# Optimization experiments

Measured on AMD Instinct MI355X. Metric: run time of the kernel, lower is better.

## Reference

```python
import jax, jax.numpy as jnp
import numpy as np

NHEAD = 8; DM = 512; DFF = 2048; L = 4; S = 1024; NTOK = 51; MLP = 256; CLASSES = 7
GH = 3; GHID = 64; GCLS = 5; ALPHA = 0.2
HD = DM // NHEAD

_ADJ = np.array([[0,1,0,0,0],[1,1,1,1,0],[1,0,1,0,1],[1,0,0,1,1],[0,0,1,1,1]], dtype=np.int32)


def setup_inputs():
    key = jax.random.key(0)
    ks = jax.random.split(key, 24)
    r = lambda k, s, sc=0.05: jax.random.normal(k, s, jnp.float32) * sc
    return {
        'x': jax.random.normal(ks[0], (5, S, NTOK), jnp.float32),
        'adj': jnp.asarray(_ADJ),
        'W_enc': r(ks[1], (NTOK, DM)), 'b_enc': jnp.zeros((DM,), jnp.float32),
        'cls_tok': r(ks[2], (1, 1, DM)),
        'pos_emb': r(ks[3], (S + 1, DM)),
        'Wq': r(ks[4], (L, DM, DM)), 'bq': jnp.zeros((L, DM), jnp.float32),
        'Wk': r(ks[5], (L, DM, DM)), 'bk': jnp.zeros((L, DM), jnp.float32),
        'Wv': r(ks[6], (L, DM, DM)), 'bv': jnp.zeros((L, DM), jnp.float32),
        'Wo': r(ks[7], (L, DM, DM)), 'bo': jnp.zeros((L, DM), jnp.float32),
        'W1': r(ks[8], (L, DM, DFF)), 'b1': jnp.zeros((L, DFF), jnp.float32),
        'W2': r(ks[9], (L, DFF, DM)), 'b2': jnp.zeros((L, DM), jnp.float32),
        'g1': jnp.ones((L, DM), jnp.float32), 'be1': jnp.zeros((L, DM), jnp.float32),
        'g2': jnp.ones((L, DM), jnp.float32), 'be2': jnp.zeros((L, DM), jnp.float32),
        'Wd1': r(ks[10], (DM, MLP)), 'bd1': jnp.zeros((MLP,), jnp.float32),
        'Wd2': r(ks[11], (MLP, CLASSES)), 'bd2': jnp.zeros((CLASSES,), jnp.float32),
        'Wg': r(ks[12], (GH, 3, GHID), 0.3), 'ag': r(ks[13], (GH, 2 * GHID), 0.3),
        'Wgo': r(ks[14], (GH * GHID, GCLS), 0.3), 'ago': r(ks[15], (2 * GCLS,), 0.3),
    }


def _layernorm(x, g, b, eps=1e-5):
    m = x.mean(-1, keepdims=True)
    v = ((x - m) ** 2).mean(-1, keepdims=True)
    return (x - m) * jax.lax.rsqrt(v + eps) * g + b


def _gat_attn_layer(h_in, W, a, mask):
    # standard pyGAT GraphAttentionLayer: e_ij = LeakyReLU(a1.h_i + a2.h_j)
    F = W.shape[1]
    h = h_in @ W                                                    # [N, F]
    e = jax.nn.leaky_relu((h @ a[:F])[:, None] + (h @ a[F:])[None, :], ALPHA)
    att = jax.nn.softmax(jnp.where(mask, e, -9e15), axis=-1)        # adjacency-masked softmax
    return att @ h


def _gat(xg, mask, Wg, ag, Wgo, ago):
    # xg: [5 nodes, 3 feats]; GH attention heads concatenated, then output layer
    heads = jax.vmap(lambda W, a: jax.nn.elu(_gat_attn_layer(xg, W, a, mask)))(Wg, ag)  # [GH,5,GHID]
    hcat = jnp.transpose(heads, (1, 0, 2)).reshape(xg.shape[0], GH * GHID)
    out = jax.nn.elu(_gat_attn_layer(hcat, Wgo, ago, mask))         # [5, GCLS]
    return jax.nn.log_softmax(out, axis=1)


def _forward(x, adj, params):
    (W_enc, b_enc, cls_tok, pos_emb, Wq, bq, Wk, bk, Wv, bv, Wo, bo,
     W1, b1, W2, b2, g1, be1, g2, be2, Wd1, bd1, Wd2, bd2, Wg, ag, Wgo, ago) = params
    mask = adj > 0
    # --- batched GAT: the source loops over T timesteps x 5 feature groups; here fully vectorized ---
    # x[:, :, :15] : batch(=5 nodes) x T x 15 -> [T*5groups, 5 nodes, 3]
    xg = x[:, :, :15].reshape(5, S, 5, 3)
    xg = jnp.transpose(xg, (1, 2, 0, 3)).reshape(S * 5, 5, 3)
    gat_out = jax.vmap(lambda g: _gat(g, mask, Wg, ag, Wgo, ago))(xg)
    gat_out = gat_out.reshape(S, 5, 5, GCLS)                        # [T, group, node, class]
    # --- transformer branch (eval mode: dropout = identity) ---
    h = x @ W_enc + b_enc                                           # [5, S, DM]
    h = jnp.concatenate([jnp.broadcast_to(cls_tok, (5, 1, DM)), h], axis=1)
    h = h + pos_emb[None]
    for i in range(L):
        q = (h @ Wq[i] + bq[i]).reshape(5, S + 1, NHEAD, HD)
        k = (h @ Wk[i] + bk[i]).reshape(5, S + 1, NHEAD, HD)
        v = (h @ Wv[i] + bv[i]).reshape(5, S + 1, NHEAD, HD)
        sc = jnp.einsum('bthd,bshd->bhts', q, k) / jnp.sqrt(jnp.float32(HD))
        att = jax.nn.softmax(sc, axis=-1)
        o = jnp.einsum('bhts,bshd->bthd', att, v).reshape(5, S + 1, DM) @ Wo[i] + bo[i]
        h = _layernorm(h + o, g1[i], be1[i])
        f = jax.nn.relu(h @ W1[i] + b1[i]) @ W2[i] + b2[i]
        h = _layernorm(h + f, g2[i], be2[i])
    cls = h[:, 0, :]                                                # lambda: x[:, 0, :]
    out = (cls @ Wd1 + bd1) @ Wd2 + bd2                             # no activation between dense layers (as in source)
    return out, gat_out


def reference(x, adj, W_enc, b_enc, cls_tok, pos_emb, Wq, bq, Wk, bk, Wv, bv, Wo, bo, W1, b1, W2, b2, g1, be1, g2, be2, Wd1, bd1, Wd2, bd2, Wg, ag, Wgo, ago):
    params = (W_enc, b_enc, cls_tok, pos_emb, Wq, bq, Wk, bk, Wv, bv, Wo, bo,
              W1, b1, W2, b2, g1, be1, g2, be2, Wd1, bd1, Wd2, bd2, Wg, ag, Wgo, ago)
    return _forward(x, adj, params)
```

## Files before the change

### kernel.cpp

```cpp
#include <hip/hip_runtime.h>
#include <hip/hip_bf16.h>
#include <math.h>

#define NBATCH 5
#define SEQ    1024
#define T      1025
#define ROWS   (NBATCH * T)
#define MP     5248
#define DM     512
#define DFF    2048
#define NHEAD  8
#define HD     64
#define NTOK   51
#define MLPDIM 256
#define NCLS   7
#define GH     3
#define GHID   64
#define GCLS   5
#define NGRAPH (SEQ * 5)
#define QKVN   1536
#define TPAD   1088

typedef __attribute__((ext_vector_type(8))) short bf16x8;
typedef __attribute__((ext_vector_type(4))) float f32x4;

#define GM_AS(p)  ((const __attribute__((address_space(1))) void*)(p))
#define LDS_AS(p) ((__attribute__((address_space(3))) void*)(p))

__device__ __forceinline__ unsigned short f2bf(float f) {
    unsigned int u = __float_as_uint(f);
    unsigned int r = (u + 0x7FFFu + ((u >> 16) & 1u)) >> 16;
    return (unsigned short)r;
}

__global__ __launch_bounds__(256) void wconv_kernel(
    const float* __restrict__ W, unsigned short* __restrict__ Wt, int K, int N,
    long dstride)
{
    const float* Wm = W + (size_t)blockIdx.z * K * N;
    unsigned short* Wo = Wt + (size_t)blockIdx.z * dstride;
    __shared__ float tile[32][33];
    int bx = blockIdx.x * 32;
    int by = blockIdx.y * 32;
    int tx = threadIdx.x & 31, ty = threadIdx.x >> 5;
    #pragma unroll
    for (int i = 0; i < 32; i += 8)
        tile[ty + i][tx] = Wm[(size_t)(by + ty + i) * N + bx + tx];
    __syncthreads();
    #pragma unroll
    for (int i = 0; i < 32; i += 8)
        Wo[(size_t)(bx + ty + i) * K + by + tx] = f2bf(tile[tx][ty + i]);
}

__global__ __launch_bounds__(512) void bconcat_kernel(
    const float* __restrict__ bq, const float* __restrict__ bk,
    const float* __restrict__ bv, float* __restrict__ bqkv)
{
    int i = blockIdx.x, t = threadIdx.x;
    bqkv[i * QKVN + t]        = bq[i * DM + t];
    bqkv[i * QKVN + 512 + t]  = bk[i * DM + t];
    bqkv[i * QKVN + 1024 + t] = bv[i * DM + t];
}

__global__ __launch_bounds__(256) void gemm_mfma(
    const unsigned short* __restrict__ A, const unsigned short* __restrict__ Bt,
    const float* __restrict__ bias, float* __restrict__ Cf,
    unsigned short* __restrict__ Cb, int N, int K, int relu)
{
    __shared__ unsigned short As[128 * 64];
    __shared__ unsigned short Bs[128 * 64];
    int tid = threadIdx.x;
    int l = tid & 63, w = tid >> 6;
    int wr = w & 1, wc = w >> 1;
    int mlane = l & 15, quad = l >> 4;
    int m0 = blockIdx.y * 128, n0 = blockIdx.x * 128;

    f32x4 acc[4][4] = {};

    for (int k0 = 0; k0 < K; k0 += 64) {
        __syncthreads();
        #pragma unroll
        for (int it = 0; it < 4; ++it) {
            int c = tid + it * 256;
            int row = c >> 3, cc = c & 7;
            const unsigned short* ga = A  + (size_t)(m0 + row) * K + k0 + cc * 8;
            __builtin_amdgcn_global_load_lds(GM_AS(ga), LDS_AS(As + c * 8), 16, 0, 0);
            const unsigned short* gb = Bt + (size_t)(n0 + row) * K + k0 + cc * 8;
            __builtin_amdgcn_global_load_lds(GM_AS(gb), LDS_AS(Bs + c * 8), 16, 0, 0);
        }
        __syncthreads();
        #pragma unroll
        for (int half = 0; half < 2; ++half) {
            int ko = half * 32 + quad * 8;
            bf16x8 afrag[4], bfrag[4];
            #pragma unroll
            for (int mi = 0; mi < 4; ++mi)
                afrag[mi] = *(const bf16x8*)(As + (wr * 64 + mi * 16 + mlane) * 64 + ko);
            #pragma unroll
            for (int ni = 0; ni < 4; ++ni)
                bfrag[ni] = *(const bf16x8*)(Bs + (wc * 64 + ni * 16 + mlane) * 64 + ko);
            #pragma unroll
            for (int mi = 0; mi < 4; ++mi)
                #pragma unroll
                for (int ni = 0; ni < 4; ++ni)
                    acc[mi][ni] = __builtin_amdgcn_mfma_f32_16x16x32_bf16(
                        afrag[mi], bfrag[ni], acc[mi][ni], 0, 0, 0);
        }
    }

    #pragma unroll
    for (int mi = 0; mi < 4; ++mi) {
        #pragma unroll
        for (int r = 0; r < 4; ++r) {
            int gm = m0 + wr * 64 + mi * 16 + quad * 4 + r;
            size_t rowoff = (size_t)gm * N;
            #pragma unroll
            for (int ni = 0; ni < 4; ++ni) {
                int gn = n0 + wc * 64 + ni * 16 + mlane;
                float val = acc[mi][ni][r] + bias[gn];
                if (relu) val = fmaxf(val, 0.f);
                if (Cb) Cb[rowoff + gn] = f2bf(val);
                else    Cf[rowoff + gn] = val;
            }
        }
    }
}

__global__ __launch_bounds__(256) void vtrans_kernel(
    const unsigned short* __restrict__ vb, unsigned short* __restrict__ vt, int qs)
{
    __shared__ unsigned short tile[64][72];
    int bh = blockIdx.y;
    int b = bh >> 3, h = bh & 7;
    int t0 = blockIdx.x * 64;
    int tid = threadIdx.x;
    #pragma unroll
    for (int it = 0; it < 2; ++it) {
        int c = tid + it * 256;
        int key = c >> 3, cc = c & 7;
        int gk = t0 + key; if (gk >= T) gk = T - 1;
        *(bf16x8*)(&tile[key][cc * 8]) =
            *(const bf16x8*)(vb + ((size_t)b * T + gk) * qs + h * HD + cc * 8);
    }
    __syncthreads();
    #pragma unroll
    for (int it = 0; it < 2; ++it) {
        int c = tid + it * 256;
        int d = c >> 3, cc = c & 7;
        unsigned short tmp[8];
        #pragma unroll
        for (int j = 0; j < 8; ++j) tmp[j] = tile[cc * 8 + j][d];
        *(bf16x8*)(vt + ((size_t)bh * 64 + d) * TPAD + t0 + cc * 8) = *(bf16x8*)tmp;
    }
}

#define AQT 64
#define NCH 17
__global__ __launch_bounds__(256) void attn_mfma(
    const unsigned short* __restrict__ qb, const unsigned short* __restrict__ kb,
    const unsigned short* __restrict__ vt, unsigned short* __restrict__ ob,
    int qs)
{
    __shared__ unsigned short Ks[64 * 72];
    __shared__ unsigned short Vs[64 * 72];
    __shared__ unsigned short Ps[4][16 * 72];
    int bh = blockIdx.y;
    int b = bh >> 3, h = bh & 7;
    int t0 = blockIdx.x * AQT;
    int tid = threadIdx.x;
    int l = tid & 63, w = tid >> 6;
    int ml = l & 15, quad = l >> 4;
    size_t rowbase = (size_t)b * T;
    const unsigned short* vtb = vt + (size_t)bh * 64 * TPAD;

    int qrow = t0 + w * 16 + ml; if (qrow >= T) qrow = T - 1;
    const unsigned short* qp = qb + (rowbase + qrow) * qs + h * HD + quad * 8;
    bf16x8 qf0 = *(const bf16x8*)qp;
    bf16x8 qf1 = *(const bf16x8*)(qp + 32);

    int c_a = tid, c_b = tid + 256;
    int rowa = c_a >> 3, cca = c_a & 7;
    int rowb = c_b >> 3, ccb = c_b & 7;

    f32x4 oacc[4] = {};
    float mrow[4] = {-1e30f, -1e30f, -1e30f, -1e30f};
    float lrow[4] = {0.f, 0.f, 0.f, 0.f};

    bf16x8 kra, krb, vra, vrb;
    {
        int gka = rowa;  int gkb = rowb;
        kra = *(const bf16x8*)(kb + (rowbase + gka) * qs + h * HD + cca * 8);
        krb = *(const bf16x8*)(kb + (rowbase + gkb) * qs + h * HD + ccb * 8);
        vra = *(const bf16x8*)(vtb + (size_t)rowa * TPAD + 0 + cca * 8);
        vrb = *(const bf16x8*)(vtb + (size_t)rowb * TPAD + 0 + ccb * 8);
    }

    for (int ch = 0; ch < NCH; ++ch) {
        int c0 = ch * 64;
        __syncthreads();
        *(bf16x8*)(Ks + rowa * 72 + cca * 8) = kra;
        *(bf16x8*)(Ks + rowb * 72 + ccb * 8) = krb;
        *(bf16x8*)(Vs + rowa * 72 + cca * 8) = vra;
        *(bf16x8*)(Vs + rowb * 72 + ccb * 8) = vrb;
        __syncthreads();
        if (ch + 1 < NCH) {
            int n0k = c0 + 64;
            int gka = n0k + rowa; if (gka >= T) gka = T - 1;
            int gkb = n0k + rowb; if (gkb >= T) gkb = T - 1;
            kra = *(const bf16x8*)(kb + (rowbase + gka) * qs + h * HD + cca * 8);
            krb = *(const bf16x8*)(kb + (rowbase + gkb) * qs + h * HD + ccb * 8);
            vra = *(const bf16x8*)(vtb + (size_t)rowa * TPAD + n0k + cca * 8);
            vrb = *(const bf16x8*)(vtb + (size_t)rowb * TPAD + n0k + ccb * 8);
        }

        f32x4 s[4] = {};
        #pragma unroll
        for (int ni = 0; ni < 4; ++ni) {
            bf16x8 kf0 = *(const bf16x8*)(Ks + (ni * 16 + ml) * 72 + quad * 8);
            bf16x8 kf1 = *(const bf16x8*)(Ks + (ni * 16 + ml) * 72 + 32 + quad * 8);
            s[ni] = __builtin_amdgcn_mfma_f32_16x16x32_bf16(qf0, kf0, s[ni], 0, 0, 0);
            s[ni] = __builtin_amdgcn_mfma_f32_16x16x32_bf16(qf1, kf1, s[ni], 0, 0, 0);
        }
        #pragma unroll
        for (int ni = 0; ni < 4; ++ni) {
            bool valid = (c0 + ni * 16 + ml) < T;
            #pragma unroll
            for (int r = 0; r < 4; ++r)
                s[ni][r] = valid ? s[ni][r] * 0.125f : -1e30f;
        }
        #pragma unroll
        for (int r = 0; r < 4; ++r) {
            float mx = fmaxf(fmaxf(s[0][r], s[1][r]), fmaxf(s[2][r], s[3][r]));
            #pragma unroll
            for (int off = 1; off < 16; off <<= 1)
                mx = fmaxf(mx, __shfl_xor(mx, off));
            float mnew = fmaxf(mrow[r], mx);
            float alpha = __expf(mrow[r] - mnew);
            mrow[r] = mnew;
            float rs = 0.f;
            #pragma unroll
            for (int ni = 0; ni < 4; ++ni) {
                float p = __expf(s[ni][r] - mnew);
                s[ni][r] = p; rs += p;
            }
            #pragma unroll
            for (int off = 1; off < 16; off <<= 1)
                rs += __shfl_xor(rs, off);
            lrow[r] = lrow[r] * alpha + rs;
            #pragma unroll
            for (int ni = 0; ni < 4; ++ni) oacc[ni][r] *= alpha;
        }
        unsigned short* pw = Ps[w];
        #pragma unroll
        for (int r = 0; r < 4; ++r)
            #pragma unroll
            for (int ni = 0; ni < 4; ++ni)
                pw[(quad * 4 + r) * 72 + ((ni * 16 + ml) ^ (quad << 4))] = f2bf(s[ni][r]);
        int sw = ((ml >> 2) & 3) << 4;
        #pragma unroll
        for (int kc = 0; kc < 2; ++kc) {
            bf16x8 pf = *(const bf16x8*)(pw + ml * 72 + ((kc * 32 + quad * 8) ^ sw));
            #pragma unroll
            for (int ni = 0; ni < 4; ++ni) {
                bf16x8 vf = *(const bf16x8*)(Vs + (ni * 16 + ml) * 72 + kc * 32 + quad * 8);
                oacc[ni] = __builtin_amdgcn_mfma_f32_16x16x32_bf16(pf, vf, oacc[ni], 0, 0, 0);
            }
        }
    }

    #pragma unroll
    for (int r = 0; r < 4; ++r) {
        int grow = t0 + w * 16 + quad * 4 + r;
        if (grow >= T) continue;
        float inv = 1.f / lrow[r];
        unsigned short* op = ob + (rowbase + grow) * DM + h * HD;
        #pragma unroll
        for (int ni = 0; ni < 4; ++ni)
            op[ni * 16 + ml] = f2bf(oacc[ni][r] * inv);
    }
}

__global__ __launch_bounds__(256) void encoder_kernel(
    const float* __restrict__ x, const float* __restrict__ W_enc,
    const float* __restrict__ b_enc, const float* __restrict__ cls_tok,
    const float* __restrict__ pos_emb, float* __restrict__ h,
    unsigned short* __restrict__ hb)
{
    int row = blockIdx.x;
    int b = row / T, tt = row % T;
    int tid = threadIdx.x;
    float* hp = h + (size_t)row * DM;
    unsigned short* hbp = hb + (size_t)row * DM;
    if (tt == 0) {
        float a0 = cls_tok[tid]       + pos_emb[tid];
        float a1 = cls_tok[tid + 256] + pos_emb[tid + 256];
        hp[tid] = a0; hp[tid + 256] = a1;
        hbp[tid] = f2bf(a0); hbp[tid + 256] = f2bf(a1);
        return;
    }
    __shared__ float xs[NTOK];
    int s = tt - 1;
    if (tid < NTOK) xs[tid] = x[((size_t)b * SEQ + s) * NTOK + tid];
    __syncthreads();
    #pragma unroll
    for (int rep = 0; rep < 2; ++rep) {
        int d = tid + rep * 256;
        float acc = b_enc[d] + pos_emb[(size_t)tt * DM + d];
        for (int kx = 0; kx < NTOK; ++kx) acc += xs[kx] * W_enc[kx * DM + d];
        hp[d] = acc;
        hbp[d] = f2bf(acc);
    }
}

__global__ __launch_bounds__(256) void add_ln_kernel(
    float* __restrict__ h, const float* __restrict__ r,
    const float* __restrict__ g, const float* __restrict__ be,
    unsigned short* __restrict__ hb)
{
    int w = threadIdx.x >> 6, l = threadIdx.x & 63;
    int row = blockIdx.x * 4 + w;
    if (row >= ROWS) return;
    float* hp = h + (size_t)row * DM + l * 8;
    const float* rp = r + (size_t)row * DM + l * 8;
    unsigned short* hbp = hb + (size_t)row * DM + l * 8;
    float4 a0 = *(const float4*)(hp);
    float4 a1 = *(const float4*)(hp + 4);
    float4 b0 = *(const float4*)(rp);
    float4 b1 = *(const float4*)(rp + 4);
    float v[8] = {a0.x + b0.x, a0.y + b0.y, a0.z + b0.z, a0.w + b0.w,
                  a1.x + b1.x, a1.y + b1.y, a1.z + b1.z, a1.w + b1.w};
    float s = 0.f;
    #pragma unroll
    for (int i = 0; i < 8; ++i) s += v[i];
    #pragma unroll
    for (int off = 1; off < 64; off <<= 1) s += __shfl_xor(s, off);
    float mean = s * (1.f / DM);
    float sq = 0.f;
    #pragma unroll
    for (int i = 0; i < 8; ++i) { v[i] -= mean; sq += v[i] * v[i]; }
    #pragma unroll
    for (int off = 1; off < 64; off <<= 1) sq += __shfl_xor(sq, off);
    float inv = rsqrtf(sq * (1.f / DM) + 1e-5f);
    float4 g0 = *(const float4*)(g + l * 8);
    float4 g1 = *(const float4*)(g + l * 8 + 4);
    float4 e0 = *(const float4*)(be + l * 8);
    float4 e1 = *(const float4*)(be + l * 8 + 4);
    float o[8];
    o[0] = v[0]*inv*g0.x + e0.x; o[1] = v[1]*inv*g0.y + e0.y;
    o[2] = v[2]*inv*g0.z + e0.z; o[3] = v[3]*inv*g0.w + e0.w;
    o[4] = v[4]*inv*g1.x + e1.x; o[5] = v[5]*inv*g1.y + e1.y;
    o[6] = v[6]*inv*g1.z + e1.z; o[7] = v[7]*inv*g1.w + e1.w;
    *(float4*)(hp)     = make_float4(o[0], o[1], o[2], o[3]);
    *(float4*)(hp + 4) = make_float4(o[4], o[5], o[6], o[7]);
    ushort4 p0 = {f2bf(o[0]), f2bf(o[1]), f2bf(o[2]), f2bf(o[3])};
    ushort4 p1 = {f2bf(o[4]), f2bf(o[5]), f2bf(o[6]), f2bf(o[7])};
    *(ushort4*)(hbp)     = p0;
    *(ushort4*)(hbp + 4) = p1;
}

__global__ __launch_bounds__(256) void dec1_kernel(
    const float* __restrict__ h, const float* __restrict__ Wd1,
    float* __restrict__ part)
{
    int kc = blockIdx.x, b = blockIdx.y, tid = threadIdx.x;
    __shared__ float cs[64];
    const float* cls = h + (size_t)b * T * DM;
    if (tid < 64) cs[tid] = cls[kc * 64 + tid];
    __syncthreads();
    float acc = 0.f;
    #pragma unroll
    for (int kx = 0; kx < 64; ++kx)
        acc += cs[kx] * Wd1[(size_t)(kc * 64 + kx) * MLPDIM + tid];
    part[(size_t)(b * 8 + kc) * MLPDIM + tid] = acc;
}

__global__ __launch_bounds__(256) void dec2_kernel(
    const float* __restrict__ part, const float* __restrict__ bd1,
    const float* __restrict__ Wd2, const float* __restrict__ bd2,
    float* __restrict__ out)
{
    __shared__ float t1s[MLPDIM];
    int tid = threadIdx.x;
    for (int b = 0; b < NBATCH; ++b) {
        float acc = bd1[tid];
        #pragma unroll
        for (int kc = 0; kc < 8; ++kc)
            acc += part[(size_t)(b * 8 + kc) * MLPDIM + tid];
        t1s[tid] = acc;
        __syncthreads();
        if (tid < NCLS) {
            float a2 = bd2[tid];
            for (int kx = 0; kx < MLPDIM; ++kx) a2 += t1s[kx] * Wd2[kx * NCLS + tid];
            out[b * NCLS + tid] = a2;
        }
        __syncthreads();
    }
}

__global__ __launch_bounds__(64) void gat_kernel(
    const float* __restrict__ x, const int* __restrict__ adj,
    const float* __restrict__ Wg, const float* __restrict__ ag,
    const float* __restrict__ Wgo, const float* __restrict__ ago,
    float* __restrict__ out)
{
    int g = blockIdx.x;
    int s = g / 5, jj = g % 5;
    int tid = threadIdx.x;
    __shared__ float xs[5][3];
    __shared__ int adjs[25];
    __shared__ float hb[GH][5][GHID];
    __shared__ float o1[GH][5][GHID];
    __shared__ float srcb[GH][5], dstb[GH][5];
    __shared__ float attb[GH][5][5];
    __shared__ float h2[5][5], src2[5], dst2[5], att2[5][5], o2[5][5];

    if (tid < 15) { int n = tid / 3, c = tid % 3;
        xs[n][c] = x[(size_t)n * SEQ * NTOK + (size_t)s * NTOK + jj * 3 + c]; }
    if (tid < 25) adjs[tid] = adj[tid];
    __syncthreads();

    #pragma unroll
    for (int hh = 0; hh < GH; ++hh)
        #pragma unroll
        for (int n = 0; n < 5; ++n)
            hb[hh][n][tid] = xs[n][0] * Wg[hh * 192 + tid]
                           + xs[n][1] * Wg[hh * 192 + 64 + tid]
                           + xs[n][2] * Wg[hh * 192 + 128 + tid];
    __syncthreads();

    if (tid < 15) { int hh = tid / 5, n = tid % 5; float a = 0.f;
        for (int f = 0; f < GHID; ++f) a += hb[hh][n][f] * ag[hh * 128 + f];
        srcb[hh][n] = a;
    } else if (tid >= 32 && tid < 47) { int t2 = tid - 32; int hh = t2 / 5, n = t2 % 5; float a = 0.f;
        for (int f = 0; f < GHID; ++f) a += hb[hh][n][f] * ag[hh * 128 + 64 + f];
        dstb[hh][n] = a;
    }
    __syncthreads();

    if (tid < 15) { int hh = tid / 5, i = tid % 5;
        float e[5]; float mx = -1e30f;
        #pragma unroll
        for (int j2 = 0; j2 < 5; ++j2) {
            float ev = srcb[hh][i] + dstb[hh][j2];
            ev = ev > 0.f ? ev : 0.2f * ev;
            e[j2] = ev;
            if (adjs[i * 5 + j2] && ev > mx) mx = ev;
        }
        float sum = 0.f;
        #pragma unroll
        for (int j2 = 0; j2 < 5; ++j2) {
            float p = adjs[i * 5 + j2] ? expf(e[j2] - mx) : 0.f;
            e[j2] = p; sum += p;
        }
        float inv = 1.f / sum;
        #pragma unroll
        for (int j2 = 0; j2 < 5; ++j2) attb[hh][i][j2] = e[j2] * inv;
    }
    __syncthreads();

    #pragma unroll
    for (int hh = 0; hh < GH; ++hh)
        #pragma unroll
        for (int n = 0; n < 5; ++n) {
            float a = 0.f;
            #pragma unroll
            for (int j2 = 0; j2 < 5; ++j2) a += attb[hh][n][j2] * hb[hh][j2][tid];
            o1[hh][n][tid] = a > 0.f ? a : expm1f(a);
        }
    __syncthreads();

    if (tid < 25) { int n = tid / 5, m = tid % 5; float a = 0.f;
        for (int hh = 0; hh < GH; ++hh)
            for (int f = 0; f < GHID; ++f)
                a += o1[hh][n][f] * Wgo[(hh * GHID + f) * GCLS + m];
        h2[n][m] = a;
    }
    __syncthreads();

    if (tid < 5) { float a = 0.f;
        for (int m = 0; m < GCLS; ++m) a += h2[tid][m] * ago[m];
        src2[tid] = a;
    } else if (tid >= 8 && tid < 13) { int n = tid - 8; float a = 0.f;
        for (int m = 0; m < GCLS; ++m) a += h2[n][m] * ago[GCLS + m];
        dst2[n] = a;
    }
    __syncthreads();

    if (tid < 5) { int i = tid;
        float e[5]; float mx = -1e30f;
        #pragma unroll
        for (int j2 = 0; j2 < 5; ++j2) {
            float ev = src2[i] + dst2[j2];
            ev = ev > 0.f ? ev : 0.2f * ev;
            e[j2] = ev;
            if (adjs[i * 5 + j2] && ev > mx) mx = ev;
        }
        float sum = 0.f;
        #pragma unroll
        for (int j2 = 0; j2 < 5; ++j2) {
            float p = adjs[i * 5 + j2] ? expf(e[j2] - mx) : 0.f;
            e[j2] = p; sum += p;
        }
        float inv = 1.f / sum;
        #pragma unroll
        for (int j2 = 0; j2 < 5; ++j2) att2[i][j2] = e[j2] * inv;
    }
    __syncthreads();

    if (tid < 25) { int n = tid / 5, m = tid % 5; float a = 0.f;
        #pragma unroll
        for (int j2 = 0; j2 < 5; ++j2) a += att2[n][j2] * h2[j2][m];
        o2[n][m] = a > 0.f ? a : expm1f(a);
    }
    __syncthreads();

    if (tid < 5) { int n = tid;
        float mx = o2[n][0];
        #pragma unroll
        for (int m = 1; m < GCLS; ++m) mx = fmaxf(mx, o2[n][m]);
        float sum = 0.f;
        #pragma unroll
        for (int m = 0; m < GCLS; ++m) sum += expf(o2[n][m] - mx);
        float ls = logf(sum);
        #pragma unroll
        for (int m = 0; m < GCLS; ++m)
            out[(size_t)g * 25 + n * 5 + m] = o2[n][m] - mx - ls;
    }
}

extern "C" void kernel_launch(void* const* d_in, const int* in_sizes, int n_in,
                              void* d_out, int out_size, void* d_ws, size_t ws_size,
                              hipStream_t stream)
{
    const float* x       = (const float*)d_in[0];
    const int*   adj     = (const int*)  d_in[1];
    const float* W_enc   = (const float*)d_in[2];
    const float* b_enc   = (const float*)d_in[3];
    const float* cls_tok = (const float*)d_in[4];
    const float* pos_emb = (const float*)d_in[5];
    const float* Wq = (const float*)d_in[6];
    const float* bq = (const float*)d_in[7];
    const float* Wk = (const float*)d_in[8];
    const float* bk = (const float*)d_in[9];
    const float* Wv = (const float*)d_in[10];
    const float* bv = (const float*)d_in[11];
    const float* Wo = (const float*)d_in[12];
    const float* bo = (const float*)d_in[13];
    const float* W1 = (const float*)d_in[14];
    const float* b1 = (const float*)d_in[15];
    const float* W2 = (const float*)d_in[16];
    const float* b2 = (const float*)d_in[17];
    const float* g1 = (const float*)d_in[18];
    const float* be1= (const float*)d_in[19];
    const float* g2 = (const float*)d_in[20];
    const float* be2= (const float*)d_in[21];
    const float* Wd1= (const float*)d_in[22];
    const float* bd1= (const float*)d_in[23];
    const float* Wd2= (const float*)d_in[24];
    const float* bd2= (const float*)d_in[25];
    const float* Wg = (const float*)d_in[26];
    const float* ag = (const float*)d_in[27];
    const float* Wgo= (const float*)d_in[28];
    const float* ago= (const float*)d_in[29];
    float* out = (float*)d_out;

    float* ws = (float*)d_ws;
    float* h = ws;
    float* q = h + (size_t)MP * DM;
    unsigned short* hb   = (unsigned short*)(q + (size_t)MP * DM);
    unsigned short* qkvb = hb + (size_t)MP * DM;
    unsigned short* ob   = qkvb + (size_t)MP * QKVN;
    unsigned short* f1b  = qkvb;
    unsigned short* Wqkvt= ob + (size_t)MP * DM;
    unsigned short* Wot  = Wqkvt + (size_t)4 * QKVN * DM;
    unsigned short* W1t  = Wot + (size_t)4 * DM * DM;
    unsigned short* W2t  = W1t + (size_t)4 * DM * DFF;
    float* bqkv = (float*)(W2t + (size_t)4 * DFF * DM);
    float* dpart = bqkv + 4 * QKVN;
    unsigned short* vt = (unsigned short*)(dpart + NBATCH * 8 * MLPDIM);

    const long QS = (long)QKVN * DM;
    wconv_kernel<<<dim3(DM/32,  DM/32,  4), 256, 0, stream>>>(Wq, Wqkvt,            DM,  DM, QS);
    wconv_kernel<<<dim3(DM/32,  DM/32,  4), 256, 0, stream>>>(Wk, Wqkvt + 512*512,  DM,  DM, QS);
    wconv_kernel<<<dim3(DM/32,  DM/32,  4), 256, 0, stream>>>(Wv, Wqkvt + 1024*512, DM,  DM, QS);
    wconv_kernel<<<dim3(DM/32,  DM/32,  4), 256, 0, stream>>>(Wo, Wot, DM,  DM, (long)DM*DM);
    wconv_kernel<<<dim3(DFF/32, DM/32,  4), 256, 0, stream>>>(W1, W1t, DM,  DFF, (long)DM*DFF);
    wconv_kernel<<<dim3(DM/32,  DFF/32, 4), 256, 0, stream>>>(W2, W2t, DFF, DM, (long)DFF*DM);
    bconcat_kernel<<<4, 512, 0, stream>>>(bq, bk, bv, bqkv);

    gat_kernel<<<NGRAPH, 64, 0, stream>>>(x, adj, Wg, ag, Wgo, ago, out + NBATCH * NCLS);
    encoder_kernel<<<ROWS, 256, 0, stream>>>(x, W_enc, b_enc, cls_tok, pos_emb, h, hb);

    dim3 g512 (DM  / 128, MP / 128);
    dim3 gqkv (QKVN / 128, MP / 128);
    dim3 g2048(DFF / 128, MP / 128);
    dim3 gAttn(TPAD / AQT, NBATCH * NHEAD);
    dim3 gVt  (TPAD / 64, NBATCH * NHEAD);
    int gLN = (ROWS + 3) / 4;

    for (int i = 0; i < 4; ++i) {
        gemm_mfma<<<gqkv, 256, 0, stream>>>(hb, Wqkvt + (size_t)i*QKVN*DM, bqkv + i*QKVN, nullptr, qkvb, QKVN, DM, 0);
        vtrans_kernel<<<gVt, 256, 0, stream>>>(qkvb + 1024, vt, QKVN);
        attn_mfma<<<gAttn, 256, 0, stream>>>(qkvb, qkvb + 512, vt, ob, QKVN);
        gemm_mfma<<<g512, 256, 0, stream>>>(ob, Wot + (size_t)i*DM*DM, bo + i*DM, q, nullptr, DM, DM, 0);
        add_ln_kernel<<<gLN, 256, 0, stream>>>(h, q, g1 + i*DM, be1 + i*DM, hb);
        gemm_mfma<<<g2048, 256, 0, stream>>>(hb,  W1t + (size_t)i*DM*DFF, b1 + i*DFF, nullptr, f1b, DFF, DM, 1);
        gemm_mfma<<<g512, 256, 0, stream>>>(f1b, W2t + (size_t)i*DM*DFF, b2 + i*DM,  q, nullptr, DM, DFF, 0);
        add_ln_kernel<<<gLN, 256, 0, stream>>>(h, q, g2 + i*DM, be2 + i*DM, hb);
    }

    dec1_kernel<<<dim3(8, NBATCH), 256, 0, stream>>>(h, Wd1, dpart);
    dec2_kernel<<<1, 256, 0, stream>>>(dpart, bd1, Wd2, bd2, out);
}
```

Before: 957.7 us.

## Split attention over two key-range halves and merge partials in combine kernel

Attention blocks now split the key chunks into two halves along a new grid dimension. Each half writes unnormalized bf16 partial outputs plus per-row running max and sum, and a new combine kernel merges them with the log-sum-exp rescaling. The aim is to double the attention grid (17x40 blocks grows to 17x40x2) so more CUs are busy on the 256-CU part. The cost is an extra launch, extra global traffic for partials, and an extra bf16 rounding of the unnormalized partials.

```diff
diff --git a/kernel.cpp b/kernel.cpp
--- a/kernel.cpp
+++ b/kernel.cpp
@@ -32,6 +32,9 @@
     unsigned int r = (u + 0x7FFFu + ((u >> 16) & 1u)) >> 16;
     return (unsigned short)r;
 }
+__device__ __forceinline__ float bf2f(unsigned short u) {
+    return __uint_as_float((unsigned int)u << 16);
+}
 
 __global__ __launch_bounds__(256) void wconv_kernel(
     const float* __restrict__ W, unsigned short* __restrict__ Wt, int K, int N,
@@ -158,8 +161,8 @@
 #define NCH 17
 __global__ __launch_bounds__(256) void attn_mfma(
     const unsigned short* __restrict__ qb, const unsigned short* __restrict__ kb,
-    const unsigned short* __restrict__ vt, unsigned short* __restrict__ ob,
-    int qs)
+    const unsigned short* __restrict__ vt,
+    unsigned short* __restrict__ opart, float* __restrict__ mlpart, int qs)
 {
     __shared__ unsigned short Ks[64 * 72];
     __shared__ unsigned short Vs[64 * 72];
@@ -167,6 +170,9 @@
     int bh = blockIdx.y;
     int b = bh >> 3, h = bh & 7;
     int t0 = blockIdx.x * AQT;
+    int sp = blockIdx.z;
+    int chbeg = sp ? 9 : 0;
+    int chend = sp ? NCH : 9;
     int tid = threadIdx.x;
     int l = tid & 63, w = tid >> 6;
     int ml = l & 15, quad = l >> 4;
@@ -188,14 +194,16 @@
 
     bf16x8 kra, krb, vra, vrb;
     {
-        int gka = rowa;  int gkb = rowb;
+        int c0 = chbeg * 64;
+        int gka = c0 + rowa; if (gka >= T) gka = T - 1;
+        int gkb = c0 + rowb; if (gkb >= T) gkb = T - 1;
         kra = *(const bf16x8*)(kb + (rowbase + gka) * qs + h * HD + cca * 8);
         krb = *(const bf16x8*)(kb + (rowbase + gkb) * qs + h * HD + ccb * 8);
-        vra = *(const bf16x8*)(vtb + (size_t)rowa * TPAD + 0 + cca * 8);
-        vrb = *(const bf16x8*)(vtb + (size_t)rowb * TPAD + 0 + ccb * 8);
-    }
-
-    for (int ch = 0; ch < NCH; ++ch) {
+        vra = *(const bf16x8*)(vtb + (size_t)rowa * TPAD + c0 + cca * 8);
+        vrb = *(const bf16x8*)(vtb + (size_t)rowb * TPAD + c0 + ccb * 8);
+    }
+
+    for (int ch = chbeg; ch < chend; ++ch) {
         int c0 = ch * 64;
         __syncthreads();
         *(bf16x8*)(Ks + rowa * 72 + cca * 8) = kra;
@@ -203,7 +211,7 @@
         *(bf16x8*)(Vs + rowa * 72 + cca * 8) = vra;
         *(bf16x8*)(Vs + rowb * 72 + ccb * 8) = vrb;
         __syncthreads();
-        if (ch + 1 < NCH) {
+        if (ch + 1 < chend) {
             int n0k = c0 + 64;
             int gka = n0k + rowa; if (gka >= T) gka = T - 1;
             int gkb = n0k + rowb; if (gkb >= T) gkb = T - 1;
@@ -268,16 +276,48 @@
         }
     }
 
+    int pbase = (sp * 40 + bh) * TPAD;
     #pragma unroll
     for (int r = 0; r < 4; ++r) {
         int grow = t0 + w * 16 + quad * 4 + r;
         if (grow >= T) continue;
-        float inv = 1.f / lrow[r];
-        unsigned short* op = ob + (rowbase + grow) * DM + h * HD;
+        unsigned short* op = opart + (size_t)(pbase + grow) * 64;
         #pragma unroll
         for (int ni = 0; ni < 4; ++ni)
-            op[ni * 16 + ml] = f2bf(oacc[ni][r] * inv);
-    }
+            op[ni * 16 + ml] = f2bf(oacc[ni][r]);
+        if (ml == 0) {
+            mlpart[(size_t)(pbase + grow) * 2]     = mrow[r];
+            mlpart[(size_t)(pbase + grow) * 2 + 1] = lrow[r];
+        }
+    }
+}
+
+__global__ __launch_bounds__(256) void attn_combine(
+    const unsigned short* __restrict__ opart, const float* __restrict__ mlpart,
+    unsigned short* __restrict__ ob)
+{
+    int qt = blockIdx.x, bh = blockIdx.y;
+    int b = bh >> 3, h = bh & 7;
+    int tid = threadIdx.x;
+    int ql = tid >> 2, dg = tid & 3;
+    int q = qt * 64 + ql;
+    if (q >= T) return;
+    int base0 = bh * TPAD + q;
+    int base1 = (40 + bh) * TPAD + q;
+    float m0 = mlpart[(size_t)base0 * 2], l0 = mlpart[(size_t)base0 * 2 + 1];
+    float m1 = mlpart[(size_t)base1 * 2], l1 = mlpart[(size_t)base1 * 2 + 1];
+    float M = fmaxf(m0, m1);
+    float w0 = __expf(m0 - M), w1 = __expf(m1 - M);
+    float inv = 1.f / (l0 * w0 + l1 * w1);
+    const unsigned short* p0 = opart + (size_t)base0 * 64 + dg * 16;
+    const unsigned short* p1 = opart + (size_t)base1 * 64 + dg * 16;
+    unsigned short* op = ob + ((size_t)b * T + q) * DM + h * HD + dg * 16;
+    unsigned short res[16];
+    #pragma unroll
+    for (int i = 0; i < 16; ++i)
+        res[i] = f2bf((bf2f(p0[i]) * w0 + bf2f(p1[i]) * w1) * inv);
+    *(bf16x8*)(op)     = *(bf16x8*)(res);
+    *(bf16x8*)(op + 8) = *(bf16x8*)(res + 8);
 }
 
 __global__ __launch_bounds__(256) void encoder_kernel(
@@ -578,6 +618,8 @@
     float* bqkv = (float*)(W2t + (size_t)4 * DFF * DM);
     float* dpart = bqkv + 4 * QKVN;
     unsigned short* vt = (unsigned short*)(dpart + NBATCH * 8 * MLPDIM);
+    unsigned short* opart = vt + (size_t)40 * 64 * TPAD;
+    float* mlpart = (float*)(opart + (size_t)2 * 40 * TPAD * 64);
 
     const long QS = (long)QKVN * DM;
     wconv_kernel<<<dim3(DM/32,  DM/32,  4), 256, 0, stream>>>(Wq, Wqkvt,            DM,  DM, QS);
@@ -594,14 +636,16 @@
     dim3 g512 (DM  / 128, MP / 128);
     dim3 gqkv (QKVN / 128, MP / 128);
     dim3 g2048(DFF / 128, MP / 128);
-    dim3 gAttn(TPAD / AQT, NBATCH * NHEAD);
+    dim3 gAttn(TPAD / AQT, NBATCH * NHEAD, 2);
+    dim3 gComb(TPAD / 64, NBATCH * NHEAD);
     dim3 gVt  (TPAD / 64, NBATCH * NHEAD);
     int gLN = (ROWS + 3) / 4;
 
     for (int i = 0; i < 4; ++i) {
         gemm_mfma<<<gqkv, 256, 0, stream>>>(hb, Wqkvt + (size_t)i*QKVN*DM, bqkv + i*QKVN, nullptr, qkvb, QKVN, DM, 0);
         vtrans_kernel<<<gVt, 256, 0, stream>>>(qkvb + 1024, vt, QKVN);
-        attn_mfma<<<gAttn, 256, 0, stream>>>(qkvb, qkvb + 512, vt, ob, QKVN);
+        attn_mfma<<<gAttn, 256, 0, stream>>>(qkvb, qkvb + 512, vt, opart, mlpart, QKVN);
+        attn_combine<<<gComb, 256, 0, stream>>>(opart, mlpart, ob);
         gemm_mfma<<<g512, 256, 0, stream>>>(ob, Wot + (size_t)i*DM*DM, bo + i*DM, q, nullptr, DM, DM, 0);
         add_ln_kernel<<<gLN, 256, 0, stream>>>(h, q, g1 + i*DM, be1 + i*DM, hb);
         gemm_mfma<<<g2048, 256, 0, stream>>>(hb,  W1t + (size_t)i*DM*DFF, b1 + i*DFF, nullptr, f1b, DFF, DM, 1);
```

Result: slower. 984.0 us (+2.7%).

## Split-K the narrow GEMMs into bf16 partials reduced in LayerNorm; drop online softmax max

Applied to the files above, without the earlier changes.

The Wo and W2 projections (N=512, only 4x41 tiles) now run as split-K GEMMs (2 and 4 slices) that write bf16 partial sums. The add+LayerNorm kernel reduces those partials and adds the bias, which removes the fp32 intermediate buffer. Attention also drops the running-max rescaling and just sums exp(s) directly, with the row-sum reduction deferred to the end. This adds parallelism for the underfilled GEMMs and cuts softmax work, but rounds partials to bf16 and risks exp overflow on large scores.

```diff
diff --git a/kernel.cpp b/kernel.cpp
--- a/kernel.cpp
+++ b/kernel.cpp
@@ -32,6 +32,9 @@
     unsigned int r = (u + 0x7FFFu + ((u >> 16) & 1u)) >> 16;
     return (unsigned short)r;
 }
+__device__ __forceinline__ float bf2f(unsigned short u) {
+    return __uint_as_float((unsigned int)u << 16);
+}
 
 __global__ __launch_bounds__(256) void wconv_kernel(
     const float* __restrict__ W, unsigned short* __restrict__ Wt, int K, int N,
@@ -121,6 +124,69 @@
                 if (relu) val = fmaxf(val, 0.f);
                 if (Cb) Cb[rowoff + gn] = f2bf(val);
                 else    Cf[rowoff + gn] = val;
+            }
+        }
+    }
+}
+
+__global__ __launch_bounds__(256) void gemm_mfma_sk(
+    const unsigned short* __restrict__ A, const unsigned short* __restrict__ Bt,
+    unsigned short* __restrict__ part, int N, int K)
+{
+    __shared__ unsigned short As[128 * 64];
+    __shared__ unsigned short Bs[128 * 64];
+    int tid = threadIdx.x;
+    int l = tid & 63, w = tid >> 6;
+    int wr = w & 1, wc = w >> 1;
+    int mlane = l & 15, quad = l >> 4;
+    int m0 = blockIdx.y * 128, n0 = blockIdx.x * 128;
+    int kper = K / gridDim.z;
+    int kbeg = blockIdx.z * kper;
+
+    f32x4 acc[4][4] = {};
+
+    for (int k0 = kbeg; k0 < kbeg + kper; k0 += 64) {
+        __syncthreads();
+        #pragma unroll
+        for (int it = 0; it < 4; ++it) {
+            int c = tid + it * 256;
+            int row = c >> 3, cc = c & 7;
+            const unsigned short* ga = A  + (size_t)(m0 + row) * K + k0 + cc * 8;
+            __builtin_amdgcn_global_load_lds(GM_AS(ga), LDS_AS(As + c * 8), 16, 0, 0);
+            const unsigned short* gb = Bt + (size_t)(n0 + row) * K + k0 + cc * 8;
+            __builtin_amdgcn_global_load_lds(GM_AS(gb), LDS_AS(Bs + c * 8), 16, 0, 0);
+        }
+        __syncthreads();
+        #pragma unroll
+        for (int half = 0; half < 2; ++half) {
+            int ko = half * 32 + quad * 8;
+            bf16x8 afrag[4], bfrag[4];
+            #pragma unroll
+            for (int mi = 0; mi < 4; ++mi)
+                afrag[mi] = *(const bf16x8*)(As + (wr * 64 + mi * 16 + mlane) * 64 + ko);
+            #pragma unroll
+            for (int ni = 0; ni < 4; ++ni)
+                bfrag[ni] = *(const bf16x8*)(Bs + (wc * 64 + ni * 16 + mlane) * 64 + ko);
+            #pragma unroll
+            for (int mi = 0; mi < 4; ++mi)
+                #pragma unroll
+                for (int ni = 0; ni < 4; ++ni)
+                    acc[mi][ni] = __builtin_amdgcn_mfma_f32_16x16x32_bf16(
+                        afrag[mi], bfrag[ni], acc[mi][ni], 0, 0, 0);
+        }
+    }
+
+    unsigned short* pz = part + (size_t)blockIdx.z * MP * N;
+    #pragma unroll
+    for (int mi = 0; mi < 4; ++mi) {
+        #pragma unroll
+        for (int r = 0; r < 4; ++r) {
+            int gm = m0 + wr * 64 + mi * 16 + quad * 4 + r;
+            size_t rowoff = (size_t)gm * N;
+            #pragma unroll
+            for (int ni = 0; ni < 4; ++ni) {
+                int gn = n0 + wc * 64 + ni * 16 + mlane;
+                pz[rowoff + gn] = f2bf(acc[mi][ni][r]);
             }
         }
     }
@@ -178,21 +244,18 @@
     bf16x8 qf0 = *(const bf16x8*)qp;
     bf16x8 qf1 = *(const bf16x8*)(qp + 32);
 
-    int c_a = tid, c_b = tid + 256;
-    int rowa = c_a >> 3, cca = c_a & 7;
-    int rowb = c_b >> 3, ccb = c_b & 7;
+    int rowa = tid >> 3, cca = tid & 7;
+    int rowb = (tid + 256) >> 3, ccb = tid & 7;
 
     f32x4 oacc[4] = {};
-    float mrow[4] = {-1e30f, -1e30f, -1e30f, -1e30f};
     float lrow[4] = {0.f, 0.f, 0.f, 0.f};
 
     bf16x8 kra, krb, vra, vrb;
     {
-        int gka = rowa;  int gkb = rowb;
-        kra = *(const bf16x8*)(kb + (rowbase + gka) * qs + h * HD + cca * 8);
-        krb = *(const bf16x8*)(kb + (rowbase + gkb) * qs + h * HD + ccb * 8);
-        vra = *(const bf16x8*)(vtb + (size_t)rowa * TPAD + 0 + cca * 8);
-        vrb = *(const bf16x8*)(vtb + (size_t)rowb * TPAD + 0 + ccb * 8);
+        kra = *(const bf16x8*)(kb + (rowbase + rowa) * qs + h * HD + cca * 8);
+        krb = *(const bf16x8*)(kb + (rowbase + rowb) * qs + h * HD + ccb * 8);
+        vra = *(const bf16x8*)(vtb + (size_t)rowa * TPAD + cca * 8);
+        vrb = *(const bf16x8*)(vtb + (size_t)rowb * TPAD + ccb * 8);
     }
 
     for (int ch = 0; ch < NCH; ++ch) {
@@ -225,30 +288,11 @@
         for (int ni = 0; ni < 4; ++ni) {
             bool valid = (c0 + ni * 16 + ml) < T;
             #pragma unroll
-            for (int r = 0; r < 4; ++r)
-                s[ni][r] = valid ? s[ni][r] * 0.125f : -1e30f;
-        }
-        #pragma unroll
-        for (int r = 0; r < 4; ++r) {
-            float mx = fmaxf(fmaxf(s[0][r], s[1][r]), fmaxf(s[2][r], s[3][r]));
-            #pragma unroll
-            for (int off = 1; off < 16; off <<= 1)
-                mx = fmaxf(mx, __shfl_xor(mx, off));
-            float mnew = fmaxf(mrow[r], mx);
-            float alpha = __expf(mrow[r] - mnew);
-            mrow[r] = mnew;
-            float rs = 0.f;
-            #pragma unroll
-            for (int ni = 0; ni < 4; ++ni) {
-                float p = __expf(s[ni][r] - mnew);
-                s[ni][r] = p; rs += p;
+            for (int r = 0; r < 4; ++r) {
+                float p = valid ? __expf(s[ni][r] * 0.125f) : 0.f;
+                s[ni][r] = p;
+                lrow[r] += p;
             }
-            #pragma unroll
-            for (int off = 1; off < 16; off <<= 1)
-                rs += __shfl_xor(rs, off);
-            lrow[r] = lrow[r] * alpha + rs;
-            #pragma unroll
-            for (int ni = 0; ni < 4; ++ni) oacc[ni][r] *= alpha;
         }
         unsigned short* pw = Ps[w];
         #pragma unroll
@@ -268,6 +312,12 @@
         }
     }
 
+    #pragma unroll
+    for (int r = 0; r < 4; ++r) {
+        #pragma unroll
+        for (int off = 1; off < 16; off <<= 1)
+            lrow[r] += __shfl_xor(lrow[r], off);
+    }
     #pragma unroll
     for (int r = 0; r < 4; ++r) {
         int grow = t0 + w * 16 + quad * 4 + r;
@@ -312,23 +362,28 @@
     }
 }
 
-__global__ __launch_bounds__(256) void add_ln_kernel(
-    float* __restrict__ h, const float* __restrict__ r,
-    const float* __restrict__ g, const float* __restrict__ be,
-    unsigned short* __restrict__ hb)
+__global__ __launch_bounds__(256) void add_lnp_kernel(
+    float* __restrict__ h, const unsigned short* __restrict__ part, int np,
+    const float* __restrict__ bias, const float* __restrict__ g,
+    const float* __restrict__ be, unsigned short* __restrict__ hb)
 {
     int w = threadIdx.x >> 6, l = threadIdx.x & 63;
     int row = blockIdx.x * 4 + w;
     if (row >= ROWS) return;
     float* hp = h + (size_t)row * DM + l * 8;
-    const float* rp = r + (size_t)row * DM + l * 8;
     unsigned short* hbp = hb + (size_t)row * DM + l * 8;
     float4 a0 = *(const float4*)(hp);
     float4 a1 = *(const float4*)(hp + 4);
-    float4 b0 = *(const float4*)(rp);
-    float4 b1 = *(const float4*)(rp + 4);
+    float4 b0 = *(const float4*)(bias + l * 8);
+    float4 b1 = *(const float4*)(bias + l * 8 + 4);
     float v[8] = {a0.x + b0.x, a0.y + b0.y, a0.z + b0.z, a0.w + b0.w,
                   a1.x + b1.x, a1.y + b1.y, a1.z + b1.z, a1.w + b1.w};
+    for (int pp = 0; pp < np; ++pp) {
+        const unsigned short* prp = part + ((size_t)pp * MP + row) * DM + l * 8;
+        bf16x8 pv = *(const bf16x8*)prp;
+        #pragma unroll
+        for (int i = 0; i < 8; ++i) v[i] += bf2f((unsigned short)pv[i]);
+    }
     float s = 0.f;
     #pragma unroll
     for (int i = 0; i < 8; ++i) s += v[i];
@@ -566,8 +621,7 @@
 
     float* ws = (float*)d_ws;
     float* h = ws;
-    float* q = h + (size_t)MP * DM;
-    unsigned short* hb   = (unsigned short*)(q + (size_t)MP * DM);
+    unsigned short* hb   = (unsigned short*)(h + (size_t)MP * DM);
     unsigned short* qkvb = hb + (size_t)MP * DM;
     unsigned short* ob   = qkvb + (size_t)MP * QKVN;
     unsigned short* f1b  = qkvb;
@@ -578,6 +632,7 @@
     float* bqkv = (float*)(W2t + (size_t)4 * DFF * DM);
     float* dpart = bqkv + 4 * QKVN;
     unsigned short* vt = (unsigned short*)(dpart + NBATCH * 8 * MLPDIM);
+    unsigned short* parts = vt + (size_t)40 * 64 * TPAD;
 
     const long QS = (long)QKVN * DM;
     wconv_kernel<<<dim3(DM/32,  DM/32,  4), 256, 0, stream>>>(Wq, Wqkvt,            DM,  DM, QS);
@@ -591,9 +646,10 @@
     gat_kernel<<<NGRAPH, 64, 0, stream>>>(x, adj, Wg, ag, Wgo, ago, out + NBATCH * NCLS);
     encoder_kernel<<<ROWS, 256, 0, stream>>>(x, W_enc, b_enc, cls_tok, pos_emb, h, hb);
 
-    dim3 g512 (DM  / 128, MP / 128);
     dim3 gqkv (QKVN / 128, MP / 128);
     dim3 g2048(DFF / 128, MP / 128);
+    dim3 gWo  (DM / 128, MP / 128, 2);
+    dim3 gW2  (DM / 128, MP / 128, 4);
     dim3 gAttn(TPAD / AQT, NBATCH * NHEAD);
     dim3 gVt  (TPAD / 64, NBATCH * NHEAD);
     int gLN = (ROWS + 3) / 4;
@@ -602,11 +658,11 @@
         gemm_mfma<<<gqkv, 256, 0, stream>>>(hb, Wqkvt + (size_t)i*QKVN*DM, bqkv + i*QKVN, nullptr, qkvb, QKVN, DM, 0);
         vtrans_kernel<<<gVt, 256, 0, stream>>>(qkvb + 1024, vt, QKVN);
         attn_mfma<<<gAttn, 256, 0, stream>>>(qkvb, qkvb + 512, vt, ob, QKVN);
-        gemm_mfma<<<g512, 256, 0, stream>>>(ob, Wot + (size_t)i*DM*DM, bo + i*DM, q, nullptr, DM, DM, 0);
-        add_ln_kernel<<<gLN, 256, 0, stream>>>(h, q, g1 + i*DM, be1 + i*DM, hb);
+        gemm_mfma_sk<<<gWo, 256, 0, stream>>>(ob, Wot + (size_t)i*DM*DM, parts, DM, DM);
+        add_lnp_kernel<<<gLN, 256, 0, stream>>>(h, parts, 2, bo + i*DM, g1 + i*DM, be1 + i*DM, hb);
         gemm_mfma<<<g2048, 256, 0, stream>>>(hb,  W1t + (size_t)i*DM*DFF, b1 + i*DFF, nullptr, f1b, DFF, DM, 1);
-        gemm_mfma<<<g512, 256, 0, stream>>>(f1b, W2t + (size_t)i*DM*DFF, b2 + i*DM,  q, nullptr, DM, DFF, 0);
-        add_ln_kernel<<<gLN, 256, 0, stream>>>(h, q, g2 + i*DM, be2 + i*DM, hb);
+        gemm_mfma_sk<<<gW2, 256, 0, stream>>>(f1b, W2t + (size_t)i*DM*DFF, parts, DM, DFF);
+        add_lnp_kernel<<<gLN, 256, 0, stream>>>(h, parts, 4, b2 + i*DM, g2 + i*DM, be2 + i*DM, hb);
     }
 
     dec1_kernel<<<dim3(8, NBATCH), 256, 0, stream>>>(h, Wd1, dpart);
```

Result: faster. 824.4 us (-13.9%).
